# Performance work log

Hardware: AMD Instinct MI355X
Metric: run time of the kernel (lower is better)

Reference implementation:

```python
import jax, jax.numpy as jnp
import numpy as np

EPS = 1e-8  # torch CosineSimilarity eps
V_FD = 2.0


def _tstudent(cos):
    # (1 + (1/v)*(1 - cos))^(-(v+1)/2)
    return (1.0 + (1.0 / V_FD) * (1.0 - cos)) ** (-(V_FD + 1.0) / 2.0)


def setup_inputs() -> dict:
    key = jax.random.key(0)
    k1, k2 = jax.random.split(key)
    z1 = jax.random.normal(k1, (8192, 768), dtype=jnp.float32)
    z2 = jax.random.normal(k2, (8192, 768), dtype=jnp.float32)
    return {"z1": z1, "z2": z2}


def reference(z1, z2):
    # L2-normalize rows (clamped norm as in torch.nn.CosineSimilarity)
    n1 = z1 / jnp.maximum(jnp.linalg.norm(z1, axis=-1, keepdims=True), EPS)
    n2 = z2 / jnp.maximum(jnp.linalg.norm(z2, axis=-1, keepdims=True), EPS)
    # full pairwise cosine matrix [N, N] computed once (replaces per-row loop)
    cos_mat = jnp.einsum('nd,md->nm', n1, n2)
    # numerator: matched-pair similarities == diagonal of cos_mat
    num = _tstudent(jnp.diagonal(cos_mat))
    # denominator: row-sum of t-Student kernel over all pairs
    denom = jnp.sum(_tstudent(cos_mat), axis=1)
    return -jnp.mean(num / denom)
```

## Files before the change

kernel.cpp:

```cpp
#include <hip/hip_runtime.h>
#include <hip/hip_bf16.h>
#include <stdint.h>

#define N_ROWS 8192
#define DIM    768
#define BM     256
#define BN     256
#define BKB    128
#define KTILES (DIM / BKB)
#define NT2    (N_ROWS / BN)
#define LDS_BYTES 131072

typedef __attribute__((ext_vector_type(4))) int   i32x4;
typedef __attribute__((ext_vector_type(4))) float f32x4;

__device__ __forceinline__ float tstudent(float c) {
    float t = 1.5f - 0.5f * c;
    float r = rsqrtf(t);
    return r * r * r;
}

__global__ __launch_bounds__(256) void norm_kernel(const float* __restrict__ z1,
                                                   const float* __restrict__ z2,
                                                   signed char* __restrict__ n1,
                                                   signed char* __restrict__ n2,
                                                   float* __restrict__ num,
                                                   float* __restrict__ inva,
                                                   float* __restrict__ invb) {
    int row = blockIdx.x;
    int t = threadIdx.x;
    const float* s1 = z1 + (size_t)row * DIM;
    const float* s2 = z2 + (size_t)row * DIM;
    float a0 = s1[t], a1 = s1[t + 256], a2 = s1[t + 512];
    float b0 = s2[t], b1 = s2[t + 256], b2 = s2[t + 512];
    float ss1 = a0 * a0 + a1 * a1 + a2 * a2;
    float ss2 = b0 * b0 + b1 * b1 + b2 * b2;
    float sd  = a0 * b0 + a1 * b1 + a2 * b2;
    for (int off = 32; off; off >>= 1) {
        ss1 += __shfl_down(ss1, off);
        ss2 += __shfl_down(ss2, off);
        sd  += __shfl_down(sd, off);
    }
    __shared__ float w1[4], w2[4], wd[4];
    __shared__ float sc1_s, sc2_s;
    if ((t & 63) == 0) { int wi = t >> 6; w1[wi] = ss1; w2[wi] = ss2; wd[wi] = sd; }
    __syncthreads();
    if (t == 0) {
        float nrm1 = fmaxf(sqrtf(w1[0] + w1[1] + w1[2] + w1[3]), 1e-8f);
        float nrm2 = fmaxf(sqrtf(w2[0] + w2[1] + w2[2] + w2[3]), 1e-8f);
        float dot  = wd[0] + wd[1] + wd[2] + wd[3];
        sc1_s = 127.0f / nrm1;
        sc2_s = 127.0f / nrm2;
        num[row] = tstudent(dot / (nrm1 * nrm2));
    }
    __syncthreads();
    float sc1 = sc1_s, sc2 = sc2_s;
    float qa0 = fminf(fmaxf(rintf(a0 * sc1), -127.f), 127.f);
    float qa1 = fminf(fmaxf(rintf(a1 * sc1), -127.f), 127.f);
    float qa2 = fminf(fmaxf(rintf(a2 * sc1), -127.f), 127.f);
    float qb0 = fminf(fmaxf(rintf(b0 * sc2), -127.f), 127.f);
    float qb1 = fminf(fmaxf(rintf(b1 * sc2), -127.f), 127.f);
    float qb2 = fminf(fmaxf(rintf(b2 * sc2), -127.f), 127.f);
    signed char* d1 = n1 + (size_t)row * DIM;
    signed char* d2 = n2 + (size_t)row * DIM;
    d1[t]       = (signed char)(int)qa0;
    d1[t + 256] = (signed char)(int)qa1;
    d1[t + 512] = (signed char)(int)qa2;
    d2[t]       = (signed char)(int)qb0;
    d2[t + 256] = (signed char)(int)qb1;
    d2[t + 512] = (signed char)(int)qb2;
    float sq1 = qa0 * qa0 + qa1 * qa1 + qa2 * qa2;
    float sq2 = qb0 * qb0 + qb1 * qb1 + qb2 * qb2;
    for (int off = 32; off; off >>= 1) {
        sq1 += __shfl_down(sq1, off);
        sq2 += __shfl_down(sq2, off);
    }
    __shared__ float wq1[4], wq2[4];
    if ((t & 63) == 0) { int wi = t >> 6; wq1[wi] = sq1; wq2[wi] = sq2; }
    __syncthreads();
    if (t == 0) {
        inva[row] = rsqrtf(wq1[0] + wq1[1] + wq1[2] + wq1[3]);
        invb[row] = rsqrtf(wq2[0] + wq2[1] + wq2[2] + wq2[3]);
    }
}


__device__ __forceinline__ void stG(const signed char* g, char* lds, int t, int j) {
    __builtin_amdgcn_global_load_lds(
        (const __attribute__((address_space(1))) void*)(g + (size_t)j * 64 * DIM),
        (__attribute__((address_space(3))) void*)(lds + t * 16 + j * 8192), 16, 0, 0);
}

#define BAR()  asm volatile("s_barrier" ::: "memory")
#define VMW(n) asm volatile("s_waitcnt vmcnt(" #n ")" ::: "memory")

#define READ_AQ(set, Abase, q)                                                  \
    set[0] = *(const i32x4*)((Abase) + rbA + ((q)*2    ) * 2048 + seg0);        \
    set[1] = *(const i32x4*)((Abase) + rbA + ((q)*2    ) * 2048 + seg1);        \
    set[2] = *(const i32x4*)((Abase) + rbA + ((q)*2 + 1) * 2048 + seg0);        \
    set[3] = *(const i32x4*)((Abase) + rbA + ((q)*2 + 1) * 2048 + seg1);

#define READ_BSEG0(dst, Bbase)                                                  \
    dst[0] = *(const i32x4*)((Bbase) + rbB + 0 * 2048 + seg0);                  \
    dst[1] = *(const i32x4*)((Bbase) + rbB + 1 * 2048 + seg0);                  \
    dst[2] = *(const i32x4*)((Bbase) + rbB + 2 * 2048 + seg0);                  \
    dst[3] = *(const i32x4*)((Bbase) + rbB + 3 * 2048 + seg0);

#define READ_BSEG1(Bbase)                                                       \
    bSeg1[0] = *(const i32x4*)((Bbase) + rbB + 0 * 2048 + seg1);                \
    bSeg1[1] = *(const i32x4*)((Bbase) + rbB + 1 * 2048 + seg1);                \
    bSeg1[2] = *(const i32x4*)((Bbase) + rbB + 2 * 2048 + seg1);                \
    bSeg1[3] = *(const i32x4*)((Bbase) + rbB + 3 * 2048 + seg1);

#define MFMA_Q(q, AS, BS0)                                                                                  \
    __builtin_amdgcn_s_setprio(1);                                                                          \
    _Pragma("unroll")                                                                                       \
    for (int n = 0; n < 4; ++n) {                                                                           \
        acc[(q)*2][n]     = __builtin_amdgcn_mfma_i32_16x16x64_i8(AS[0], BS0[n], acc[(q)*2][n], 0, 0, 0);       \
        acc[(q)*2][n]     = __builtin_amdgcn_mfma_i32_16x16x64_i8(AS[1], bSeg1[n], acc[(q)*2][n], 0, 0, 0);     \
        acc[(q)*2 + 1][n] = __builtin_amdgcn_mfma_i32_16x16x64_i8(AS[2], BS0[n], acc[(q)*2 + 1][n], 0, 0, 0);   \
        acc[(q)*2 + 1][n] = __builtin_amdgcn_mfma_i32_16x16x64_i8(AS[3], bSeg1[n], acc[(q)*2 + 1][n], 0, 0, 0); \
    }                                                                                                       \
    __builtin_amdgcn_s_setprio(0);

#define TILE(kt, B0c, B0n, PAR)                                                 \
    {                                                                           \
        const char* Ab  = smem + (PAR) * 32768;                                 \
        const char* Bb  = smem + 65536 + (PAR) * 32768;                         \
        const char* AbN = smem + ((PAR) ^ 1) * 32768;                           \
        const char* BbN = smem + 65536 + ((PAR) ^ 1) * 32768;                   \
        char* AnW = smem + ((PAR) ^ 1) * 32768;                                 \
        char* BnW = smem + 65536 + ((PAR) ^ 1) * 32768;                         \
        const signed char* Agn = Ag + ((kt) + 1) * BKB;                         \
        const signed char* Bgn = Bg + ((kt) + 1) * BKB;                         \
                                                                       \
        stG(Bgn, BnW, t, 0); stG(Bgn, BnW, t, 1);                               \
        READ_BSEG1(Bb);                                                         \
        READ_AQ(aS1, Ab, 1);                                                    \
        MFMA_Q(0, aS0, B0c);                                                    \
                                                                       \
        stG(Bgn, BnW, t, 2); stG(Bgn, BnW, t, 3);                               \
        VMW(4); BAR();                                                          \
        READ_AQ(aS0, Ab, 2);                                                    \
        MFMA_Q(1, aS1, B0c);                                                    \
                                                                       \
        stG(Agn, AnW, t, 0); stG(Agn, AnW, t, 2);                               \
        READ_AQ(aS1, Ab, 3);                                                    \
        MFMA_Q(2, aS0, B0c);                                                    \
                                                                       \
        stG(Agn, AnW, t, 1); stG(Agn, AnW, t, 3);                               \
        VMW(2); BAR();                                                          \
        READ_BSEG0(B0n, BbN);                                                   \
        READ_AQ(aS0, AbN, 0);                                                   \
        MFMA_Q(3, aS1, B0c);                                                    \
    }

__global__ __launch_bounds__(512, 2) void gemm_kernel(const signed char* __restrict__ n1,
                                                      const signed char* __restrict__ n2,
                                                      const float* __restrict__ inva,
                                                      const float* __restrict__ invb,
                                                      float* __restrict__ partial) {
    extern __shared__ char smem[];
    int t = threadIdx.x;
    int l = t & 63;
    int w = t >> 6;
    int wr = w >> 2;
    int wc = w & 3;

    int bid = blockIdx.x;
    int xcd = bid & 7, idx = bid >> 3;
    int br = xcd * 4 + (idx & 3);
    int bc = (idx >> 4) * 4 + ((idx >> 2) & 3);
    int rowbase = br * BM, colbase = bc * BN;

    int sr = t >> 3;
    int gcol0 = ((t & 7) ^ (sr & 7)) * 16;
    const signed char* Ag = n1 + (size_t)(rowbase + sr) * DIM + gcol0;
    const signed char* Bg = n2 + (size_t)(colbase + sr) * DIM + gcol0;

    i32x4 acc[8][4] = {};

    int seg0 = (((l >> 4) + 0) ^ (l & 7)) * 16;
    int seg1 = (((l >> 4) + 4) ^ (l & 7)) * 16;
    int rbA = (wr * 128 + (l & 15)) * 128;
    int rbB = (wc * 64 + (l & 15)) * 128;

    i32x4 aS0[4], aS1[4];
    i32x4 bB0s0[4], bB1s0[4];
    i32x4 bSeg1[4];

    {
        char* A0b = smem;
        char* B0b = smem + 65536;
        stG(Bg, B0b, t, 0); stG(Bg, B0b, t, 1); stG(Bg, B0b, t, 2); stG(Bg, B0b, t, 3);
        stG(Ag, A0b, t, 0); stG(Ag, A0b, t, 2); stG(Ag, A0b, t, 1); stG(Ag, A0b, t, 3);
    }
    VMW(2);
    BAR();
    READ_BSEG0(bB0s0, smem + 65536);
    READ_AQ(aS0, smem, 0);

    TILE(0, bB0s0, bB1s0, 0)
    TILE(1, bB1s0, bB0s0, 1)
    TILE(2, bB0s0, bB1s0, 0)
    TILE(3, bB1s0, bB0s0, 1)
    TILE(4, bB0s0, bB1s0, 0)
    {
        const char* Ab = smem + 32768;
        const char* Bb = smem + 65536 + 32768;
        READ_BSEG1(Bb);
        READ_AQ(aS1, Ab, 1);
        MFMA_Q(0, aS0, bB1s0);
        VMW(0); BAR();
        READ_AQ(aS0, Ab, 2);
        MFMA_Q(1, aS1, bB1s0);
        READ_AQ(aS1, Ab, 3);
        MFMA_Q(2, aS0, bB1s0);
        MFMA_Q(3, aS1, bB1s0);
    }

    float invb_n[4];
    #pragma unroll
    for (int n = 0; n < 4; ++n)
        invb_n[n] = invb[colbase + wc * 64 + n * 16 + (l & 15)];

    float* red = (float*)smem;
    __syncthreads();
    #pragma unroll
    for (int m = 0; m < 8; ++m) {
        f32x4 ia = *(const f32x4*)(inva + rowbase + wr * 128 + m * 16 + (l >> 4) * 4);
        #pragma unroll
        for (int j = 0; j < 4; ++j) {
            float s = 0.f;
            #pragma unroll
            for (int n = 0; n < 4; ++n) {
                float cos = (float)acc[m][n][j] * ia[j] * invb_n[n];
                s += tstudent(cos);
            }
            s += __shfl_xor(s, 1);
            s += __shfl_xor(s, 2);
            s += __shfl_xor(s, 4);
            s += __shfl_xor(s, 8);
            if ((l & 15) == 0) {
                int row = wr * 128 + m * 16 + (l >> 4) * 4 + j;
                red[row * 4 + wc] = s;
            }
        }
    }
    __syncthreads();
    if (t < BM) {
        partial[(size_t)bc * N_ROWS + rowbase + t] = red[t * 4 + 0] + red[t * 4 + 1] + red[t * 4 + 2] + red[t * 4 + 3];
    }
}

__global__ __launch_bounds__(256) void reduce_kernel(const float* __restrict__ partial,
                                                     const float* __restrict__ num,
                                                     float* __restrict__ blocksum) {
    int row = blockIdx.x * 256 + threadIdx.x;
    float d = 0.f;
    #pragma unroll 8
    for (int ct = 0; ct < NT2; ++ct) d += partial[(size_t)ct * N_ROWS + row];
    float s = num[row] / d;
    for (int off = 32; off; off >>= 1) s += __shfl_down(s, off);
    __shared__ float wsum[4];
    if ((threadIdx.x & 63) == 0) wsum[threadIdx.x >> 6] = s;
    __syncthreads();
    if (threadIdx.x == 0) blocksum[blockIdx.x] = wsum[0] + wsum[1] + wsum[2] + wsum[3];
}

__global__ __launch_bounds__(64) void final_kernel(const float* __restrict__ blocksum,
                                                   float* __restrict__ out) {
    int l = threadIdx.x;
    float s = (l < 32) ? blocksum[l] : 0.f;
    for (int off = 32; off; off >>= 1) s += __shfl_down(s, off);
    if (l == 0) out[0] = -(s / (float)N_ROWS);
}

extern "C" void kernel_launch(void* const* d_in, const int* in_sizes, int n_in,
                              void* d_out, int out_size, void* d_ws, size_t ws_size,
                              hipStream_t stream) {
    const float* z1 = (const float*)d_in[0];
    const float* z2 = (const float*)d_in[1];
    char* ws = (char*)d_ws;
    const size_t n_bytes = (size_t)N_ROWS * DIM;
    signed char* n1 = (signed char*)ws;
    signed char* n2 = (signed char*)(ws + n_bytes);
    size_t base2 = 2 * n_bytes;
    float* num      = (float*)(ws + base2);
    float* inva     = (float*)(ws + base2 + 32768);
    float* invb     = (float*)(ws + base2 + 65536);
    float* partial  = (float*)(ws + base2 + 98304);
    float* blocksum = (float*)(ws + base2 + 98304 + 2097152);

    hipFuncSetAttribute((const void*)gemm_kernel,
                        hipFuncAttributeMaxDynamicSharedMemorySize, LDS_BYTES);

    norm_kernel<<<N_ROWS, 256, 0, stream>>>(z1, z2, n1, n2, num, inva, invb);
    gemm_kernel<<<NT2 * NT2, 512, LDS_BYTES, stream>>>(n1, n2, inva, invb, partial);
    reduce_kernel<<<N_ROWS / 256, 256, 0, stream>>>(partial, num, blocksum);
    final_kernel<<<1, 64, 0, stream>>>(blocksum, (float*)d_out);
}
```

Before: 95.30 us.

## Switch GEMM to 16 waves per block with a simple double-buffered k-loop

Each 256x256 GEMM block now launches 1024 threads, so each wave computes a 64x64 sub-tile instead of 128x64. The hand-interleaved TILE macro pipeline is replaced by a plain loop that issues the next k-tile's global-to-LDS loads, computes the current tile, then waits for all loads and synchronises. The goal is to hide latency through more resident waves and fewer accumulator registers per wave rather than through manual scheduling. In exchange, each MFMA needs more LDS reads, and the full vmcnt(0) wait plus barrier every iteration removes the previous fine-grained overlap.

New measurement: 90.08 us. -5.5%, faster.

```diff
diff --git a/kernel.cpp b/kernel.cpp
--- a/kernel.cpp
+++ b/kernel.cpp
@@ -11,8 +11,8 @@
 #define NT2    (N_ROWS / BN)
 #define LDS_BYTES 131072
 
-typedef __attribute__((ext_vector_type(4))) int   i32x4;
-typedef __attribute__((ext_vector_type(4))) float f32x4;
+typedef __attribute__((ext_vector_type(4)))  int   i32x4;
+typedef __attribute__((ext_vector_type(4)))  float f32x4;
 
 __device__ __forceinline__ float tstudent(float c) {
     float t = 1.5f - 0.5f * c;
@@ -87,79 +87,43 @@
 
 __device__ __forceinline__ void stG(const signed char* g, char* lds, int t, int j) {
     __builtin_amdgcn_global_load_lds(
-        (const __attribute__((address_space(1))) void*)(g + (size_t)j * 64 * DIM),
-        (__attribute__((address_space(3))) void*)(lds + t * 16 + j * 8192), 16, 0, 0);
+        (const __attribute__((address_space(1))) void*)(g + (size_t)j * 128 * DIM),
+        (__attribute__((address_space(3))) void*)(lds + t * 16 + j * 16384), 16, 0, 0);
 }
 
 #define BAR()  asm volatile("s_barrier" ::: "memory")
 #define VMW(n) asm volatile("s_waitcnt vmcnt(" #n ")" ::: "memory")
 
-#define READ_AQ(set, Abase, q)                                                  \
-    set[0] = *(const i32x4*)((Abase) + rbA + ((q)*2    ) * 2048 + seg0);        \
-    set[1] = *(const i32x4*)((Abase) + rbA + ((q)*2    ) * 2048 + seg1);        \
-    set[2] = *(const i32x4*)((Abase) + rbA + ((q)*2 + 1) * 2048 + seg0);        \
-    set[3] = *(const i32x4*)((Abase) + rbA + ((q)*2 + 1) * 2048 + seg1);
-
-#define READ_BSEG0(dst, Bbase)                                                  \
-    dst[0] = *(const i32x4*)((Bbase) + rbB + 0 * 2048 + seg0);                  \
-    dst[1] = *(const i32x4*)((Bbase) + rbB + 1 * 2048 + seg0);                  \
-    dst[2] = *(const i32x4*)((Bbase) + rbB + 2 * 2048 + seg0);                  \
-    dst[3] = *(const i32x4*)((Bbase) + rbB + 3 * 2048 + seg0);
-
-#define READ_BSEG1(Bbase)                                                       \
-    bSeg1[0] = *(const i32x4*)((Bbase) + rbB + 0 * 2048 + seg1);                \
-    bSeg1[1] = *(const i32x4*)((Bbase) + rbB + 1 * 2048 + seg1);                \
-    bSeg1[2] = *(const i32x4*)((Bbase) + rbB + 2 * 2048 + seg1);                \
-    bSeg1[3] = *(const i32x4*)((Bbase) + rbB + 3 * 2048 + seg1);
-
-#define MFMA_Q(q, AS, BS0)                                                                                  \
-    __builtin_amdgcn_s_setprio(1);                                                                          \
-    _Pragma("unroll")                                                                                       \
-    for (int n = 0; n < 4; ++n) {                                                                           \
-        acc[(q)*2][n]     = __builtin_amdgcn_mfma_i32_16x16x64_i8(AS[0], BS0[n], acc[(q)*2][n], 0, 0, 0);       \
-        acc[(q)*2][n]     = __builtin_amdgcn_mfma_i32_16x16x64_i8(AS[1], bSeg1[n], acc[(q)*2][n], 0, 0, 0);     \
-        acc[(q)*2 + 1][n] = __builtin_amdgcn_mfma_i32_16x16x64_i8(AS[2], BS0[n], acc[(q)*2 + 1][n], 0, 0, 0);   \
-        acc[(q)*2 + 1][n] = __builtin_amdgcn_mfma_i32_16x16x64_i8(AS[3], bSeg1[n], acc[(q)*2 + 1][n], 0, 0, 0); \
-    }                                                                                                       \
-    __builtin_amdgcn_s_setprio(0);
-
-#define TILE(kt, B0c, B0n, PAR)                                                 \
-    {                                                                           \
-        const char* Ab  = smem + (PAR) * 32768;                                 \
-        const char* Bb  = smem + 65536 + (PAR) * 32768;                         \
-        const char* AbN = smem + ((PAR) ^ 1) * 32768;                           \
-        const char* BbN = smem + 65536 + ((PAR) ^ 1) * 32768;                   \
-        char* AnW = smem + ((PAR) ^ 1) * 32768;                                 \
-        char* BnW = smem + 65536 + ((PAR) ^ 1) * 32768;                         \
-        const signed char* Agn = Ag + ((kt) + 1) * BKB;                         \
-        const signed char* Bgn = Bg + ((kt) + 1) * BKB;                         \
-                                                                       \
-        stG(Bgn, BnW, t, 0); stG(Bgn, BnW, t, 1);                               \
-        READ_BSEG1(Bb);                                                         \
-        READ_AQ(aS1, Ab, 1);                                                    \
-        MFMA_Q(0, aS0, B0c);                                                    \
-                                                                       \
-        stG(Bgn, BnW, t, 2); stG(Bgn, BnW, t, 3);                               \
-        VMW(4); BAR();                                                          \
-        READ_AQ(aS0, Ab, 2);                                                    \
-        MFMA_Q(1, aS1, B0c);                                                    \
-                                                                       \
-        stG(Agn, AnW, t, 0); stG(Agn, AnW, t, 2);                               \
-        READ_AQ(aS1, Ab, 3);                                                    \
-        MFMA_Q(2, aS0, B0c);                                                    \
-                                                                       \
-        stG(Agn, AnW, t, 1); stG(Agn, AnW, t, 3);                               \
-        VMW(2); BAR();                                                          \
-        READ_BSEG0(B0n, BbN);                                                   \
-        READ_AQ(aS0, AbN, 0);                                                   \
-        MFMA_Q(3, aS1, B0c);                                                    \
-    }
-
-__global__ __launch_bounds__(512, 2) void gemm_kernel(const signed char* __restrict__ n1,
-                                                      const signed char* __restrict__ n2,
-                                                      const float* __restrict__ inva,
-                                                      const float* __restrict__ invb,
-                                                      float* __restrict__ partial) {
+#define HALF(mq)                                                                                      \
+    {                                                                                                 \
+        i32x4 a00 = *(const i32x4*)(Ab + rbA + ((mq)    ) * 2048 + seg0);                             \
+        i32x4 a01 = *(const i32x4*)(Ab + rbA + ((mq)    ) * 2048 + seg1);                             \
+        i32x4 a10 = *(const i32x4*)(Ab + rbA + ((mq) + 1) * 2048 + seg0);                             \
+        i32x4 a11 = *(const i32x4*)(Ab + rbA + ((mq) + 1) * 2048 + seg1);                             \
+        __builtin_amdgcn_s_setprio(1);                                                                \
+        _Pragma("unroll")                                                                             \
+        for (int n = 0; n < 4; ++n) {                                                                 \
+            acc[(mq)][n]     = __builtin_amdgcn_mfma_i32_16x16x64_i8(a00, bS0[n], acc[(mq)][n], 0, 0, 0);     \
+            acc[(mq)][n]     = __builtin_amdgcn_mfma_i32_16x16x64_i8(a01, bS1[n], acc[(mq)][n], 0, 0, 0);     \
+            acc[(mq) + 1][n] = __builtin_amdgcn_mfma_i32_16x16x64_i8(a10, bS0[n], acc[(mq) + 1][n], 0, 0, 0); \
+            acc[(mq) + 1][n] = __builtin_amdgcn_mfma_i32_16x16x64_i8(a11, bS1[n], acc[(mq) + 1][n], 0, 0, 0); \
+        }                                                                                             \
+        __builtin_amdgcn_s_setprio(0);                                                                \
+    }
+
+#define READ_B()                                                                \
+    i32x4 bS0[4], bS1[4];                                                       \
+    _Pragma("unroll")                                                           \
+    for (int n = 0; n < 4; ++n) {                                               \
+        bS0[n] = *(const i32x4*)(Bb + rbB + n * 2048 + seg0);                   \
+        bS1[n] = *(const i32x4*)(Bb + rbB + n * 2048 + seg1);                   \
+    }
+
+__global__ __launch_bounds__(1024) void gemm_kernel(const signed char* __restrict__ n1,
+                                                    const signed char* __restrict__ n2,
+                                                    const float* __restrict__ inva,
+                                                    const float* __restrict__ invb,
+                                                    float* __restrict__ partial) {
     extern __shared__ char smem[];
     int t = threadIdx.x;
     int l = t & 63;
@@ -178,45 +142,39 @@
     const signed char* Ag = n1 + (size_t)(rowbase + sr) * DIM + gcol0;
     const signed char* Bg = n2 + (size_t)(colbase + sr) * DIM + gcol0;
 
-    i32x4 acc[8][4] = {};
+    i32x4 acc[4][4] = {};
 
     int seg0 = (((l >> 4) + 0) ^ (l & 7)) * 16;
     int seg1 = (((l >> 4) + 4) ^ (l & 7)) * 16;
-    int rbA = (wr * 128 + (l & 15)) * 128;
+    int rbA = (wr * 64 + (l & 15)) * 128;
     int rbB = (wc * 64 + (l & 15)) * 128;
 
-    i32x4 aS0[4], aS1[4];
-    i32x4 bB0s0[4], bB1s0[4];
-    i32x4 bSeg1[4];
-
-    {
-        char* A0b = smem;
-        char* B0b = smem + 65536;
-        stG(Bg, B0b, t, 0); stG(Bg, B0b, t, 1); stG(Bg, B0b, t, 2); stG(Bg, B0b, t, 3);
-        stG(Ag, A0b, t, 0); stG(Ag, A0b, t, 2); stG(Ag, A0b, t, 1); stG(Ag, A0b, t, 3);
-    }
-    VMW(2);
-    BAR();
-    READ_BSEG0(bB0s0, smem + 65536);
-    READ_AQ(aS0, smem, 0);
-
-    TILE(0, bB0s0, bB1s0, 0)
-    TILE(1, bB1s0, bB0s0, 1)
-    TILE(2, bB0s0, bB1s0, 0)
-    TILE(3, bB1s0, bB0s0, 1)
-    TILE(4, bB0s0, bB1s0, 0)
+    stG(Ag, smem, t, 0);         stG(Ag, smem, t, 1);
+    stG(Bg, smem + 65536, t, 0); stG(Bg, smem + 65536, t, 1);
+    VMW(0); BAR();
+
+    for (int kt = 0; kt < KTILES - 1; ++kt) {
+        int db = kt & 1;
+        const char* Ab = smem + db * 32768;
+        const char* Bb = smem + 65536 + db * 32768;
+        char* AnW = smem + (db ^ 1) * 32768;
+        char* BnW = smem + 65536 + (db ^ 1) * 32768;
+        const signed char* Agn = Ag + (kt + 1) * BKB;
+        const signed char* Bgn = Bg + (kt + 1) * BKB;
+
+        stG(Agn, AnW, t, 0); stG(Agn, AnW, t, 1);
+        stG(Bgn, BnW, t, 0); stG(Bgn, BnW, t, 1);
+        READ_B();
+        HALF(0);
+        HALF(2);
+        VMW(0); BAR();
+    }
     {
         const char* Ab = smem + 32768;
         const char* Bb = smem + 65536 + 32768;
-        READ_BSEG1(Bb);
-        READ_AQ(aS1, Ab, 1);
-        MFMA_Q(0, aS0, bB1s0);
-        VMW(0); BAR();
-        READ_AQ(aS0, Ab, 2);
-        MFMA_Q(1, aS1, bB1s0);
-        READ_AQ(aS1, Ab, 3);
-        MFMA_Q(2, aS0, bB1s0);
-        MFMA_Q(3, aS1, bB1s0);
+        READ_B();
+        HALF(0);
+        HALF(2);
     }
 
     float invb_n[4];
@@ -227,8 +185,8 @@
     float* red = (float*)smem;
     __syncthreads();
     #pragma unroll
-    for (int m = 0; m < 8; ++m) {
-        f32x4 ia = *(const f32x4*)(inva + rowbase + wr * 128 + m * 16 + (l >> 4) * 4);
+    for (int m = 0; m < 4; ++m) {
+        f32x4 ia = *(const f32x4*)(inva + rowbase + wr * 64 + m * 16 + (l >> 4) * 4);
         #pragma unroll
         for (int j = 0; j < 4; ++j) {
             float s = 0.f;
@@ -242,7 +200,7 @@
             s += __shfl_xor(s, 4);
             s += __shfl_xor(s, 8);
             if ((l & 15) == 0) {
-                int row = wr * 128 + m * 16 + (l >> 4) * 4 + j;
+                int row = wr * 64 + m * 16 + (l >> 4) * 4 + j;
                 red[row * 4 + wc] = s;
             }
         }
@@ -296,7 +254,7 @@
                         hipFuncAttributeMaxDynamicSharedMemorySize, LDS_BYTES);
 
     norm_kernel<<<N_ROWS, 256, 0, stream>>>(z1, z2, n1, n2, num, inva, invb);
-    gemm_kernel<<<NT2 * NT2, 512, LDS_BYTES, stream>>>(n1, n2, inva, invb, partial);
+    gemm_kernel<<<NT2 * NT2, 1024, LDS_BYTES, stream>>>(n1, n2, inva, invb, partial);
     reduce_kernel<<<N_ROWS / 256, 256, 0, stream>>>(partial, num, blocksum);
     final_kernel<<<1, 64, 0, stream>>>(blocksum, (float*)d_out);
 }
```
